# Performance work log

Hardware: AMD Instinct MI355X
Metric: run time of the kernel (lower is better)

Reference implementation:

```python
import jax, jax.numpy as jnp
import numpy as np

B, N = 32, 512            # batch, max nodes per graph
F_DIM, M_DIM = 1024, 256  # node feature dim, first hidden dim
N_SEM = 8                 # number of semantic-class experts
XYZ, DIM_E = 3, 8
OUT_SIZE = 2 * XYZ + DIM_E  # 14 (default reg branch)
EPS = 1e-8                # padding value used by out_seq_to_batch


def setup_inputs() -> dict:
    key = jax.random.key(0)
    ks = jax.random.split(key, 12)
    def w(k, shape, fan_in):
        return jax.random.normal(k, shape, jnp.float32) / np.float32(np.sqrt(fan_in))
    return {
        "nodes": jax.random.normal(ks[0], (B, N, F_DIM), jnp.float32),
        "sem": jax.random.randint(ks[1], (B, N), 0, N_SEM, jnp.int32),
        "lengths": jax.random.randint(ks[2], (B,), 64, N + 1, jnp.int32),
        # y expert MLPs (4 layers), stacked over experts
        "W1": w(ks[3], (N_SEM, F_DIM, M_DIM), F_DIM), "b1": jnp.zeros((N_SEM, M_DIM), jnp.float32),
        "W2": w(ks[4], (N_SEM, M_DIM, 64), M_DIM),   "b2": jnp.zeros((N_SEM, 64), jnp.float32),
        "W3": w(ks[5], (N_SEM, 64, 32), 64),         "b3": jnp.zeros((N_SEM, 32), jnp.float32),
        "W4": w(ks[6], (N_SEM, 32, OUT_SIZE), 32),   "b4": jnp.zeros((N_SEM, OUT_SIZE), jnp.float32),
        # rot expert MLPs (2 layers), stacked over experts
        "R1": w(ks[7], (N_SEM, F_DIM, M_DIM), F_DIM), "rb1": jnp.zeros((N_SEM, M_DIM), jnp.float32),
        "R2": w(ks[8], (N_SEM, M_DIM, XYZ), M_DIM),   "rb2": jnp.zeros((N_SEM, XYZ), jnp.float32),
    }


def _prim_mlps(nodes, sem, lengths, W1, b1, W2, b2, W3, b3, W4, b4, R1, rb1, R2, rb2):
    Bn, Nn, Fd = nodes.shape
    x = nodes.reshape(-1, Fd)                       # [T, F], T = B*N tokens
    semf = sem.reshape(-1)                          # [T] expert id per token
    # dense dispatch: run every expert on all tokens, then select per token
    h1 = jax.nn.relu(jnp.einsum('tf,efm->etm', x, W1) + b1[:, None, :])   # [E,T,M]
    h2 = jax.nn.relu(jnp.einsum('etm,emh->eth', h1, W2) + b2[:, None, :]) # [E,T,64]
    h3 = jax.nn.relu(jnp.einsum('eth,ehg->etg', h2, W3) + b3[:, None, :]) # [E,T,32]
    y_all = jnp.einsum('etg,ego->eto', h3, W4) + b4[:, None, :]           # [E,T,OUT]
    r1 = jax.nn.relu(jnp.einsum('tf,efm->etm', x, R1) + rb1[:, None, :])  # [E,T,M]
    rot_all = jnp.einsum('etm,emo->eto', r1, R2) + rb2[:, None, :]        # [E,T,XYZ]
    t = jnp.arange(x.shape[0])
    y = y_all[semf, t]                              # [T, OUT]
    rot = rot_all[semf, t]                          # [T, XYZ]
    out = jnp.concatenate([y, rot], axis=-1).reshape(Bn, Nn, -1)
    # positions beyond each graph's length are filled with eps (out_seq_to_batch)
    mask = (jnp.arange(Nn)[None, :] < lengths[:, None])[:, :, None]
    return jnp.where(mask, out, jnp.float32(EPS))


def reference(nodes, sem, lengths, W1, b1, W2, b2, W3, b3, W4, b4, R1, rb1, R2, rb2):
    return _prim_mlps(nodes, sem, lengths, W1, b1, W2, b2, W3, b3, W4, b4,
                      R1, rb1, R2, rb2)
```

## Files before the change

### kernel.cpp

```cpp
#include <hip/hip_runtime.h>
#include <stdint.h>

#define T_TOK 16384
#define NE 8
#define EPSV 1e-8f
#define MAXC128 136
#define MAXC64  264

#define WS_PERM   0
#define WS_PART   65536
#define WS_OFFS   67584
#define WS_XS     131072
#define WS_WT     (WS_XS + 16512*1024*2)
#define WS_H1     (WS_WT + 8*512*1024*2)
#define WS_W2T    (WS_H1 + 16448*512*2)
#define WS_W3T    (WS_W2T + 8*64*256*2)
#define WS_W4T    (WS_W3T + 8*32*64*2)
#define WS_R2T    (WS_W4T + 8*16*32*2)

typedef __attribute__((ext_vector_type(8))) short bf16x8;
typedef __attribute__((ext_vector_type(4))) float f32x4;

__device__ __forceinline__ unsigned short f2bf(float f) {
    unsigned u = __float_as_uint(f);
    u += 0x7fffu + ((u >> 16) & 1u);
    return (unsigned short)(u >> 16);
}
__device__ __forceinline__ float bf2f(unsigned short h) {
    return __uint_as_float(((unsigned)h) << 16);
}

__device__ __forceinline__ void gl_lds16(const void* g, void* l) {
    __builtin_amdgcn_global_load_lds(
        (const __attribute__((address_space(1))) void*)g,
        (__attribute__((address_space(3))) void*)l,
        16, 0, 0);
}

__device__ __forceinline__ bool chunk_lookup(const int* __restrict__ offs, int c, int csize,
                                             int& e, int& base, int& len) {
    int acc = 0;
#pragma unroll
    for (int i = 0; i < NE; i++) {
        int s = offs[i], t = offs[i + 1];
        int cc = (t - s + csize - 1) / csize;
        if (c < acc + cc) {
            e = i;
            base = s + (c - acc) * csize;
            len = (t - base < csize) ? (t - base) : csize;
            return true;
        }
        acc += cc;
    }
    return false;
}

__global__ __launch_bounds__(256) void k_hist(const int* __restrict__ sem, int* __restrict__ ws_i) {
    __shared__ int cnt[NE];
    int tid = threadIdx.x, lane = tid & 63;
    if (tid < NE) cnt[tid] = 0;
    __syncthreads();
    int s = sem[blockIdx.x * 256 + tid];
#pragma unroll
    for (int e = 0; e < NE; e++) {
        unsigned long long m = __ballot(s == e);
        if (lane == e) atomicAdd(&cnt[e], (int)__popcll(m));
    }
    __syncthreads();
    if (tid < NE) ws_i[(WS_PART >> 2) + blockIdx.x * NE + tid] = cnt[tid];
}

__global__ __launch_bounds__(256) void k_scatter(const int* __restrict__ sem, int* __restrict__ ws_i) {
    __shared__ int parts[64 * NE];
    __shared__ int tot[NE], preb[NE], ebase[NE + 1];
    __shared__ int cur[NE];
    int b = blockIdx.x, tid = threadIdx.x, lane = tid & 63;
    parts[tid] = ws_i[(WS_PART >> 2) + tid];
    parts[256 + tid] = ws_i[(WS_PART >> 2) + 256 + tid];
    __syncthreads();
    if (tid < NE) {
        int t = 0, p = 0;
        for (int bb = 0; bb < 64; bb++) {
            int v = parts[bb * NE + tid];
            t += v;
            if (bb < b) p += v;
        }
        tot[tid] = t; preb[tid] = p;
    }
    __syncthreads();
    if (tid == 0) {
        int base = 0;
        for (int e = 0; e < NE; e++) { ebase[e] = base; base += tot[e]; }
        ebase[NE] = base;
        if (b == 0)
            for (int e = 0; e <= NE; e++) ws_i[(WS_OFFS >> 2) + e] = ebase[e];
    }
    __syncthreads();
    if (tid < NE) cur[tid] = ebase[tid] + preb[tid];
    __syncthreads();
    int i = b * 256 + tid;
    int s = sem[i];
    int* perm = ws_i + (WS_PERM >> 2);
#pragma unroll
    for (int e = 0; e < NE; e++) {
        unsigned long long m = __ballot(s == e);
        if (s == e) {
            int leader = (int)__builtin_ctzll(m);
            int rank = (int)__popcll(m & ((1ull << lane) - 1ull));
            int bpos = 0;
            if (lane == leader) bpos = atomicAdd(&cur[e], (int)__popcll(m));
            bpos = __shfl(bpos, leader, 64);
            perm[bpos + rank] = i;
        }
    }
}

__global__ __launch_bounds__(256) void k_xgather(const float* __restrict__ x,
                                                 const int* __restrict__ perm,
                                                 unsigned short* __restrict__ xs) {
    int gid = blockIdx.x * 256 + threadIdx.x;
    int st = gid >> 7;
    int k8 = gid & 127;
    int src = perm[st];
    const float4* p = (const float4*)(x + (size_t)src * 1024 + k8 * 8);
    float4 a = p[0], b = p[1];
    unsigned r0 = (unsigned)f2bf(a.x) | ((unsigned)f2bf(a.y) << 16);
    unsigned r1 = (unsigned)f2bf(a.z) | ((unsigned)f2bf(a.w) << 16);
    unsigned r2 = (unsigned)f2bf(b.x) | ((unsigned)f2bf(b.y) << 16);
    unsigned r3 = (unsigned)f2bf(b.z) | ((unsigned)f2bf(b.w) << 16);
    *(uint4*)(xs + (size_t)st * 1024 + k8 * 8) = make_uint4(r0, r1, r2, r3);
}

__global__ __launch_bounds__(256) void k_wcvt(const float* __restrict__ W1,
                                              const float* __restrict__ R1,
                                              const float* __restrict__ W2,
                                              const float* __restrict__ W3,
                                              const float* __restrict__ W4,
                                              const float* __restrict__ R2,
                                              unsigned short* __restrict__ wt,
                                              unsigned short* __restrict__ w2t,
                                              unsigned short* __restrict__ w3t,
                                              unsigned short* __restrict__ w4t,
                                              unsigned short* __restrict__ r2t) {
    __shared__ float tile[64][65];
    int k0 = blockIdx.x * 64;
    int n0 = blockIdx.y * 64;
    int e  = blockIdx.z;
    const float* src = (n0 < 256) ? (W1 + (size_t)e * 1024 * 256 + n0)
                                  : (R1 + (size_t)e * 1024 * 256 + (n0 - 256));
    int tid = threadIdx.x;
    int rr = tid >> 4;
    int cg = (tid & 15) * 4;
#pragma unroll
    for (int p = 0; p < 4; p++) {
        int kk = p * 16 + rr;
        float4 v = *(const float4*)(src + (size_t)(k0 + kk) * 256 + cg);
        tile[kk][cg] = v.x; tile[kk][cg + 1] = v.y; tile[kk][cg + 2] = v.z; tile[kk][cg + 3] = v.w;
    }
    __syncthreads();
    int nn = tid >> 3;
    int k8 = tid & 7;
#pragma unroll
    for (int p = 0; p < 2; p++) {
        int n = p * 32 + nn;
        unsigned w[4];
#pragma unroll
        for (int j = 0; j < 4; j++) {
            float f0 = tile[k8 * 8 + 2 * j][n];
            float f1 = tile[k8 * 8 + 2 * j + 1][n];
            w[j] = (unsigned)f2bf(f0) | ((unsigned)f2bf(f1) << 16);
        }
        *(uint4*)(wt + (size_t)(e * 512 + n0 + n) * 1024 + k0 + k8 * 8) =
            make_uint4(w[0], w[1], w[2], w[3]);
    }
    if (blockIdx.y == 0) {
        int x = blockIdx.x;
        for (int j = tid; j < 1024; j += 256) {
            int idx = x * 1024 + j; int k = idx & 255, n = idx >> 8;
            w2t[(size_t)(e * 64 + n) * 256 + k] = f2bf(W2[(size_t)e * 16384 + k * 64 + n]);
        }
        if (tid < 128) {
            int idx = x * 128 + tid; int k = idx & 63, n = idx >> 6;
            w3t[(size_t)(e * 32 + n) * 64 + k] = f2bf(W3[(size_t)e * 2048 + k * 32 + n]);
        }
        if (tid < 32) {
            int idx = x * 32 + tid; int k = idx & 31, n = idx >> 5;
            w4t[(size_t)(e * 16 + n) * 32 + k] = (n < 14) ? f2bf(W4[(size_t)e * 448 + k * 14 + n])
                                                          : (unsigned short)0;
        }
        {
            int idx = x * 256 + tid; int k = idx & 255, n = idx >> 8;
            r2t[(size_t)(e * 16 + n) * 256 + k] = (n < 3) ? f2bf(R2[(size_t)e * 768 + k * 3 + n])
                                                          : (unsigned short)0;
        }
    }
}

__global__ __launch_bounds__(256) void k_gemm(const unsigned short* __restrict__ xs,
                                              const unsigned short* __restrict__ wt,
                                              const float* __restrict__ b1,
                                              const float* __restrict__ rb1,
                                              const int* __restrict__ ws_i,
                                              unsigned short* __restrict__ h1) {
    __shared__ __align__(16) short As[128 * 64];
    __shared__ __align__(16) short Bs[128 * 64];
    int e, base, len;
    if (!chunk_lookup(ws_i + (WS_OFFS >> 2), blockIdx.x, 128, e, base, len)) return;
    int n0 = blockIdx.y * 128;
    int tid = threadIdx.x;
    int wave = tid >> 6, lane = tid & 63;
    int quad = lane >> 4, lr = lane & 15;
    int wm = (wave & 1) * 64, wn = (wave >> 1) * 64;

    f32x4 acc[4][4];
#pragma unroll
    for (int i = 0; i < 4; i++)
#pragma unroll
        for (int j = 0; j < 4; j++) acc[i][j] = (f32x4){0.f, 0.f, 0.f, 0.f};

    const unsigned short* Ag = xs + (size_t)base * 1024;
    const unsigned short* Bg = wt + (size_t)(e * 512 + n0) * 1024;

    const unsigned short* srcA[4];
    const unsigned short* srcB[4];
    int dst[4];
#pragma unroll
    for (int i = 0; i < 4; i++) {
        int s = i * 256 + wave * 64 + lane;
        int r = s >> 3, c = s & 7;
        int cs = c ^ (r & 7);
        srcA[i] = Ag + (size_t)r * 1024 + cs * 8;
        srcB[i] = Bg + (size_t)r * 1024 + cs * 8;
        dst[i] = (i * 256 + wave * 64) * 8;
    }

    for (int kb = 0; kb < 16; kb++) {
        __syncthreads();
#pragma unroll
        for (int i = 0; i < 4; i++) {
            gl_lds16(srcA[i] + kb * 64, As + dst[i]);
            gl_lds16(srcB[i] + kb * 64, Bs + dst[i]);
        }
        __syncthreads();

        bf16x8 af[2][4], bfr[2][4];
#pragma unroll
        for (int im = 0; im < 4; im++) {
            int r = wm + im * 16 + lr;
#pragma unroll
            for (int kh = 0; kh < 2; kh++) {
                int q = kh * 4 + quad;
                af[kh][im] = *(const bf16x8*)(As + (r * 8 + (q ^ (r & 7))) * 8);
            }
        }
#pragma unroll
        for (int in = 0; in < 4; in++) {
            int r = wn + in * 16 + lr;
#pragma unroll
            for (int kh = 0; kh < 2; kh++) {
                int q = kh * 4 + quad;
                bfr[kh][in] = *(const bf16x8*)(Bs + (r * 8 + (q ^ (r & 7))) * 8);
            }
        }
#pragma unroll
        for (int kh = 0; kh < 2; kh++)
#pragma unroll
            for (int im = 0; im < 4; im++)
#pragma unroll
                for (int in = 0; in < 4; in++)
                    acc[im][in] = __builtin_amdgcn_mfma_f32_16x16x32_bf16(af[kh][im], bfr[kh][in], acc[im][in], 0, 0, 0);
    }

#pragma unroll
    for (int in = 0; in < 4; in++) {
        int gcol = n0 + wn + in * 16 + lr;
        float bias = (gcol < 256) ? b1[e * 256 + gcol] : rb1[e * 256 + gcol - 256];
#pragma unroll
        for (int im = 0; im < 4; im++) {
#pragma unroll
            for (int v = 0; v < 4; v++) {
                int r = wm + im * 16 + quad * 4 + v;
                if (r < len) {
                    float val = fmaxf(acc[im][in][v] + bias, 0.f);
                    h1[(size_t)(base + r) * 512 + gcol] = f2bf(val);
                }
            }
        }
    }
}

__global__ __launch_bounds__(256) void k_tail(const unsigned short* __restrict__ h1,
                                              const int* __restrict__ ws_i,
                                              const unsigned short* __restrict__ w2t,
                                              const unsigned short* __restrict__ w3t,
                                              const unsigned short* __restrict__ w4t,
                                              const unsigned short* __restrict__ r2t,
                                              const float* __restrict__ b2,
                                              const float* __restrict__ b3,
                                              const float* __restrict__ b4,
                                              const float* __restrict__ rb2,
                                              const int* __restrict__ lengths,
                                              float* __restrict__ out) {
    __shared__ __align__(16) unsigned short h2s[4][16][64];
    __shared__ __align__(16) unsigned short h3s[4][16][32];

    int e, base, len;
    if (!chunk_lookup(ws_i + (WS_OFFS >> 2), blockIdx.x, 64, e, base, len)) return;
    int tid = threadIdx.x, wave = tid >> 6, lane = tid & 63;
    int quad = lane >> 4, lr = lane & 15;
    int m0 = wave * 16;

    const unsigned short* Ap = h1 + (size_t)(base + m0) * 512;

    f32x4 acc2[4];
#pragma unroll
    for (int t = 0; t < 4; t++) {
        float bb = b2[e * 64 + t * 16 + lr];
        acc2[t] = (f32x4){bb, bb, bb, bb};
    }
    f32x4 accr;
    { float bb = (lr < 3) ? rb2[e * 3 + lr] : 0.f; accr = (f32x4){bb, bb, bb, bb}; }

    const unsigned short* W2e = w2t + (size_t)e * 64 * 256;
    const unsigned short* R2e = r2t + (size_t)e * 16 * 256;
#pragma unroll
    for (int kk = 0; kk < 8; kk++) {
        int k0 = kk * 32;
        bf16x8 a = *(const bf16x8*)(Ap + lr * 512 + k0 + quad * 8);
#pragma unroll
        for (int t = 0; t < 4; t++) {
            bf16x8 b = *(const bf16x8*)(W2e + (t * 16 + lr) * 256 + k0 + quad * 8);
            acc2[t] = __builtin_amdgcn_mfma_f32_16x16x32_bf16(a, b, acc2[t], 0, 0, 0);
        }
        bf16x8 ar = *(const bf16x8*)(Ap + lr * 512 + 256 + k0 + quad * 8);
        bf16x8 br = *(const bf16x8*)(R2e + lr * 256 + k0 + quad * 8);
        accr = __builtin_amdgcn_mfma_f32_16x16x32_bf16(ar, br, accr, 0, 0, 0);
    }
#pragma unroll
    for (int t = 0; t < 4; t++)
#pragma unroll
        for (int v = 0; v < 4; v++)
            h2s[wave][quad * 4 + v][t * 16 + lr] = f2bf(fmaxf(acc2[t][v], 0.f));

    f32x4 acc3[2];
#pragma unroll
    for (int t = 0; t < 2; t++) {
        float bb = b3[e * 32 + t * 16 + lr];
        acc3[t] = (f32x4){bb, bb, bb, bb};
    }
    const unsigned short* W3e = w3t + (size_t)e * 32 * 64;
#pragma unroll
    for (int kk = 0; kk < 2; kk++) {
        int k0 = kk * 32;
        bf16x8 a = *(const bf16x8*)(&h2s[wave][lr][k0 + quad * 8]);
#pragma unroll
        for (int t = 0; t < 2; t++) {
            bf16x8 b = *(const bf16x8*)(W3e + (t * 16 + lr) * 64 + k0 + quad * 8);
            acc3[t] = __builtin_amdgcn_mfma_f32_16x16x32_bf16(a, b, acc3[t], 0, 0, 0);
        }
    }
#pragma unroll
    for (int t = 0; t < 2; t++)
#pragma unroll
        for (int v = 0; v < 4; v++)
            h3s[wave][quad * 4 + v][t * 16 + lr] = f2bf(fmaxf(acc3[t][v], 0.f));

    f32x4 acc4;
    { float bb = (lr < 14) ? b4[e * 14 + lr] : 0.f; acc4 = (f32x4){bb, bb, bb, bb}; }
    {
        bf16x8 a = *(const bf16x8*)(&h3s[wave][lr][quad * 8]);
        bf16x8 b = *(const bf16x8*)(w4t + ((size_t)e * 16 + lr) * 32 + quad * 8);
        acc4 = __builtin_amdgcn_mfma_f32_16x16x32_bf16(a, b, acc4, 0, 0, 0);
    }

    const int* perm = ws_i + (WS_PERM >> 2);
#pragma unroll
    for (int v = 0; v < 4; v++) {
        int t = m0 + quad * 4 + v;
        if (t < len) {
            int token = perm[base + t];
            int bi = token >> 9, ni = token & 511;
            int valid = ni < lengths[bi];
            if (lr < 14) out[(size_t)token * 17 + lr] = valid ? acc4[v] : EPSV;
            if (lr < 3)  out[(size_t)token * 17 + 14 + lr] = valid ? accr[v] : EPSV;
        }
    }
}

extern "C" void kernel_launch(void* const* d_in, const int* in_sizes, int n_in,
                              void* d_out, int out_size, void* d_ws, size_t ws_size,
                              hipStream_t stream) {
    (void)in_sizes; (void)n_in; (void)out_size; (void)ws_size;
    const float* nodes   = (const float*)d_in[0];
    const int*   sem     = (const int*)d_in[1];
    const int*   lengths = (const int*)d_in[2];
    const float* W1 = (const float*)d_in[3];
    const float* b1 = (const float*)d_in[4];
    const float* W2 = (const float*)d_in[5];
    const float* b2 = (const float*)d_in[6];
    const float* W3 = (const float*)d_in[7];
    const float* b3 = (const float*)d_in[8];
    const float* W4 = (const float*)d_in[9];
    const float* b4 = (const float*)d_in[10];
    const float* R1  = (const float*)d_in[11];
    const float* rb1 = (const float*)d_in[12];
    const float* R2  = (const float*)d_in[13];
    const float* rb2 = (const float*)d_in[14];
    float* out = (float*)d_out;

    char* ws = (char*)d_ws;
    int* ws_i = (int*)ws;
    unsigned short* xs  = (unsigned short*)(ws + WS_XS);
    unsigned short* wt  = (unsigned short*)(ws + WS_WT);
    unsigned short* h1  = (unsigned short*)(ws + WS_H1);
    unsigned short* w2t = (unsigned short*)(ws + WS_W2T);
    unsigned short* w3t = (unsigned short*)(ws + WS_W3T);
    unsigned short* w4t = (unsigned short*)(ws + WS_W4T);
    unsigned short* r2t = (unsigned short*)(ws + WS_R2T);

    hipLaunchKernelGGL(k_hist, dim3(64), dim3(256), 0, stream, sem, ws_i);
    hipLaunchKernelGGL(k_scatter, dim3(64), dim3(256), 0, stream, sem, ws_i);
    hipLaunchKernelGGL(k_xgather, dim3(8192), dim3(256), 0, stream, nodes, (const int*)ws_i, xs);
    hipLaunchKernelGGL(k_wcvt, dim3(16, 8, 8), dim3(256), 0, stream,
                       W1, R1, W2, W3, W4, R2, wt, w2t, w3t, w4t, r2t);
    hipLaunchKernelGGL(k_gemm, dim3(MAXC128, 4), dim3(256), 0, stream,
                       (const unsigned short*)xs, (const unsigned short*)wt, b1, rb1,
                       (const int*)ws_i, h1);
    hipLaunchKernelGGL(k_tail, dim3(MAXC64), dim3(256), 0, stream,
                       (const unsigned short*)h1, (const int*)ws_i,
                       (const unsigned short*)w2t, (const unsigned short*)w3t,
                       (const unsigned short*)w4t, (const unsigned short*)r2t,
                       b2, b3, b4, rb2, lengths, out);
}
```

Before: 204.2 us.

## Fuse token gather and bf16 conversion into GEMM A-tile loads; merge prep kernels

Drops the separate gather kernel, which wrote a permuted bf16 copy of the node features. The first-layer GEMM now reads fp32 rows straight from the input through the permutation, converts them to bf16 in registers and stores them into LDS. The histogram and weight-conversion kernels are merged into one launch, so there are fewer launches and the 32MB intermediate write and reread are gone. The cost is that each of the 4 N-tile blocks re-reads the fp32 A rows, doubling A bytes per load compared with bf16. A is now loaded synchronously through registers instead of asynchronously with global_load_lds.

Result: slower. 213.4 us (+4.5%).

```diff
diff --git a/kernel.cpp b/kernel.cpp
--- a/kernel.cpp
+++ b/kernel.cpp
@@ -10,8 +10,7 @@
 #define WS_PERM   0
 #define WS_PART   65536
 #define WS_OFFS   67584
-#define WS_XS     131072
-#define WS_WT     (WS_XS + 16512*1024*2)
+#define WS_WT     131072
 #define WS_H1     (WS_WT + 8*512*1024*2)
 #define WS_W2T    (WS_H1 + 16448*512*2)
 #define WS_W3T    (WS_W2T + 8*64*256*2)
@@ -25,9 +24,6 @@
     unsigned u = __float_as_uint(f);
     u += 0x7fffu + ((u >> 16) & 1u);
     return (unsigned short)(u >> 16);
-}
-__device__ __forceinline__ float bf2f(unsigned short h) {
-    return __uint_as_float(((unsigned)h) << 16);
 }
 
 __device__ __forceinline__ void gl_lds16(const void* g, void* l) {
@@ -55,19 +51,86 @@
     return false;
 }
 
-__global__ __launch_bounds__(256) void k_hist(const int* __restrict__ sem, int* __restrict__ ws_i) {
-    __shared__ int cnt[NE];
-    int tid = threadIdx.x, lane = tid & 63;
-    if (tid < NE) cnt[tid] = 0;
+__global__ __launch_bounds__(256) void k_prep1(const float* __restrict__ W1,
+                                               const float* __restrict__ R1,
+                                               const float* __restrict__ W2,
+                                               const float* __restrict__ W3,
+                                               const float* __restrict__ W4,
+                                               const float* __restrict__ R2,
+                                               const int* __restrict__ sem,
+                                               unsigned short* __restrict__ wt,
+                                               unsigned short* __restrict__ w2t,
+                                               unsigned short* __restrict__ w3t,
+                                               unsigned short* __restrict__ w4t,
+                                               unsigned short* __restrict__ r2t,
+                                               int* __restrict__ ws_i) {
+    __shared__ float tile[64][65];
+    int id = blockIdx.x, tid = threadIdx.x;
+    if (id >= 1024) {
+        __shared__ int cnt[NE];
+        int hb = id - 1024, lane = tid & 63;
+        if (tid < NE) cnt[tid] = 0;
+        __syncthreads();
+        int s = sem[hb * 256 + tid];
+#pragma unroll
+        for (int e = 0; e < NE; e++) {
+            unsigned long long m = __ballot(s == e);
+            if (lane == e) atomicAdd(&cnt[e], (int)__popcll(m));
+        }
+        __syncthreads();
+        if (tid < NE) ws_i[(WS_PART >> 2) + hb * NE + tid] = cnt[tid];
+        return;
+    }
+    int e = id >> 7, rem = id & 127;
+    int ny = rem >> 4, kx = rem & 15;
+    int k0 = kx * 64, n0 = ny * 64;
+    const float* src = (n0 < 256) ? (W1 + (size_t)e * 1024 * 256 + n0)
+                                  : (R1 + (size_t)e * 1024 * 256 + (n0 - 256));
+    int rr = tid >> 4;
+    int cg = (tid & 15) * 4;
+#pragma unroll
+    for (int p = 0; p < 4; p++) {
+        int kk = p * 16 + rr;
+        float4 v = *(const float4*)(src + (size_t)(k0 + kk) * 256 + cg);
+        tile[kk][cg] = v.x; tile[kk][cg + 1] = v.y; tile[kk][cg + 2] = v.z; tile[kk][cg + 3] = v.w;
+    }
     __syncthreads();
-    int s = sem[blockIdx.x * 256 + tid];
-#pragma unroll
-    for (int e = 0; e < NE; e++) {
-        unsigned long long m = __ballot(s == e);
-        if (lane == e) atomicAdd(&cnt[e], (int)__popcll(m));
-    }
-    __syncthreads();
-    if (tid < NE) ws_i[(WS_PART >> 2) + blockIdx.x * NE + tid] = cnt[tid];
+    int nn = tid >> 3;
+    int k8 = tid & 7;
+#pragma unroll
+    for (int p = 0; p < 2; p++) {
+        int n = p * 32 + nn;
+        unsigned w[4];
+#pragma unroll
+        for (int j = 0; j < 4; j++) {
+            float f0 = tile[k8 * 8 + 2 * j][n];
+            float f1 = tile[k8 * 8 + 2 * j + 1][n];
+            w[j] = (unsigned)f2bf(f0) | ((unsigned)f2bf(f1) << 16);
+        }
+        *(uint4*)(wt + (size_t)(e * 512 + n0 + n) * 1024 + k0 + k8 * 8) =
+            make_uint4(w[0], w[1], w[2], w[3]);
+    }
+    if (ny == 0) {
+        int x = kx;
+        for (int j = tid; j < 1024; j += 256) {
+            int idx = x * 1024 + j; int k = idx & 255, n = idx >> 8;
+            w2t[(size_t)(e * 64 + n) * 256 + k] = f2bf(W2[(size_t)e * 16384 + k * 64 + n]);
+        }
+        if (tid < 128) {
+            int idx = x * 128 + tid; int k = idx & 63, n = idx >> 6;
+            w3t[(size_t)(e * 32 + n) * 64 + k] = f2bf(W3[(size_t)e * 2048 + k * 32 + n]);
+        }
+        if (tid < 32) {
+            int idx = x * 32 + tid; int k = idx & 31, n = idx >> 5;
+            w4t[(size_t)(e * 16 + n) * 32 + k] = (n < 14) ? f2bf(W4[(size_t)e * 448 + k * 14 + n])
+                                                          : (unsigned short)0;
+        }
+        {
+            int idx = x * 256 + tid; int k = idx & 255, n = idx >> 8;
+            r2t[(size_t)(e * 16 + n) * 256 + k] = (n < 3) ? f2bf(R2[(size_t)e * 768 + k * 3 + n])
+                                                          : (unsigned short)0;
+        }
+    }
 }
 
 __global__ __launch_bounds__(256) void k_scatter(const int* __restrict__ sem, int* __restrict__ ws_i) {
@@ -115,88 +178,7 @@
     }
 }
 
-__global__ __launch_bounds__(256) void k_xgather(const float* __restrict__ x,
-                                                 const int* __restrict__ perm,
-                                                 unsigned short* __restrict__ xs) {
-    int gid = blockIdx.x * 256 + threadIdx.x;
-    int st = gid >> 7;
-    int k8 = gid & 127;
-    int src = perm[st];
-    const float4* p = (const float4*)(x + (size_t)src * 1024 + k8 * 8);
-    float4 a = p[0], b = p[1];
-    unsigned r0 = (unsigned)f2bf(a.x) | ((unsigned)f2bf(a.y) << 16);
-    unsigned r1 = (unsigned)f2bf(a.z) | ((unsigned)f2bf(a.w) << 16);
-    unsigned r2 = (unsigned)f2bf(b.x) | ((unsigned)f2bf(b.y) << 16);
-    unsigned r3 = (unsigned)f2bf(b.z) | ((unsigned)f2bf(b.w) << 16);
-    *(uint4*)(xs + (size_t)st * 1024 + k8 * 8) = make_uint4(r0, r1, r2, r3);
-}
-
-__global__ __launch_bounds__(256) void k_wcvt(const float* __restrict__ W1,
-                                              const float* __restrict__ R1,
-                                              const float* __restrict__ W2,
-                                              const float* __restrict__ W3,
-                                              const float* __restrict__ W4,
-                                              const float* __restrict__ R2,
-                                              unsigned short* __restrict__ wt,
-                                              unsigned short* __restrict__ w2t,
-                                              unsigned short* __restrict__ w3t,
-                                              unsigned short* __restrict__ w4t,
-                                              unsigned short* __restrict__ r2t) {
-    __shared__ float tile[64][65];
-    int k0 = blockIdx.x * 64;
-    int n0 = blockIdx.y * 64;
-    int e  = blockIdx.z;
-    const float* src = (n0 < 256) ? (W1 + (size_t)e * 1024 * 256 + n0)
-                                  : (R1 + (size_t)e * 1024 * 256 + (n0 - 256));
-    int tid = threadIdx.x;
-    int rr = tid >> 4;
-    int cg = (tid & 15) * 4;
-#pragma unroll
-    for (int p = 0; p < 4; p++) {
-        int kk = p * 16 + rr;
-        float4 v = *(const float4*)(src + (size_t)(k0 + kk) * 256 + cg);
-        tile[kk][cg] = v.x; tile[kk][cg + 1] = v.y; tile[kk][cg + 2] = v.z; tile[kk][cg + 3] = v.w;
-    }
-    __syncthreads();
-    int nn = tid >> 3;
-    int k8 = tid & 7;
-#pragma unroll
-    for (int p = 0; p < 2; p++) {
-        int n = p * 32 + nn;
-        unsigned w[4];
-#pragma unroll
-        for (int j = 0; j < 4; j++) {
-            float f0 = tile[k8 * 8 + 2 * j][n];
-            float f1 = tile[k8 * 8 + 2 * j + 1][n];
-            w[j] = (unsigned)f2bf(f0) | ((unsigned)f2bf(f1) << 16);
-        }
-        *(uint4*)(wt + (size_t)(e * 512 + n0 + n) * 1024 + k0 + k8 * 8) =
-            make_uint4(w[0], w[1], w[2], w[3]);
-    }
-    if (blockIdx.y == 0) {
-        int x = blockIdx.x;
-        for (int j = tid; j < 1024; j += 256) {
-            int idx = x * 1024 + j; int k = idx & 255, n = idx >> 8;
-            w2t[(size_t)(e * 64 + n) * 256 + k] = f2bf(W2[(size_t)e * 16384 + k * 64 + n]);
-        }
-        if (tid < 128) {
-            int idx = x * 128 + tid; int k = idx & 63, n = idx >> 6;
-            w3t[(size_t)(e * 32 + n) * 64 + k] = f2bf(W3[(size_t)e * 2048 + k * 32 + n]);
-        }
-        if (tid < 32) {
-            int idx = x * 32 + tid; int k = idx & 31, n = idx >> 5;
-            w4t[(size_t)(e * 16 + n) * 32 + k] = (n < 14) ? f2bf(W4[(size_t)e * 448 + k * 14 + n])
-                                                          : (unsigned short)0;
-        }
-        {
-            int idx = x * 256 + tid; int k = idx & 255, n = idx >> 8;
-            r2t[(size_t)(e * 16 + n) * 256 + k] = (n < 3) ? f2bf(R2[(size_t)e * 768 + k * 3 + n])
-                                                          : (unsigned short)0;
-        }
-    }
-}
-
-__global__ __launch_bounds__(256) void k_gemm(const unsigned short* __restrict__ xs,
+__global__ __launch_bounds__(256) void k_gemm(const float* __restrict__ nodes,
                                               const unsigned short* __restrict__ wt,
                                               const float* __restrict__ b1,
                                               const float* __restrict__ rb1,
@@ -211,6 +193,7 @@
     int wave = tid >> 6, lane = tid & 63;
     int quad = lane >> 4, lr = lane & 15;
     int wm = (wave & 1) * 64, wn = (wave >> 1) * 64;
+    const int* perm = ws_i + (WS_PERM >> 2);
 
     f32x4 acc[4][4];
 #pragma unroll
@@ -218,28 +201,38 @@
 #pragma unroll
         for (int j = 0; j < 4; j++) acc[i][j] = (f32x4){0.f, 0.f, 0.f, 0.f};
 
-    const unsigned short* Ag = xs + (size_t)base * 1024;
     const unsigned short* Bg = wt + (size_t)(e * 512 + n0) * 1024;
 
-    const unsigned short* srcA[4];
+    int cs = (tid & 7) ^ ((tid >> 3) & 7);
+    const float* srcA[4];
     const unsigned short* srcB[4];
-    int dst[4];
+    int dstA[4], dstB[4];
 #pragma unroll
     for (int i = 0; i < 4; i++) {
+        int R = i * 32 + (tid >> 3);
+        int row = base + R; if (row > T_TOK - 1) row = T_TOK - 1;
+        srcA[i] = nodes + (size_t)perm[row] * 1024 + cs * 8;
+        dstA[i] = (i * 256 + tid) * 8;
         int s = i * 256 + wave * 64 + lane;
-        int r = s >> 3, c = s & 7;
-        int cs = c ^ (r & 7);
-        srcA[i] = Ag + (size_t)r * 1024 + cs * 8;
-        srcB[i] = Bg + (size_t)r * 1024 + cs * 8;
-        dst[i] = (i * 256 + wave * 64) * 8;
+        int r = s >> 3, cb = (s & 7) ^ (r & 7);
+        srcB[i] = Bg + (size_t)r * 1024 + cb * 8;
+        dstB[i] = (i * 256 + wave * 64) * 8;
     }
 
     for (int kb = 0; kb < 16; kb++) {
         __syncthreads();
 #pragma unroll
+        for (int i = 0; i < 4; i++)
+            gl_lds16(srcB[i] + kb * 64, Bs + dstB[i]);
+#pragma unroll
         for (int i = 0; i < 4; i++) {
-            gl_lds16(srcA[i] + kb * 64, As + dst[i]);
-            gl_lds16(srcB[i] + kb * 64, Bs + dst[i]);
+            const float4* p = (const float4*)(srcA[i] + kb * 64);
+            float4 a = p[0], b = p[1];
+            unsigned r0 = (unsigned)f2bf(a.x) | ((unsigned)f2bf(a.y) << 16);
+            unsigned r1 = (unsigned)f2bf(a.z) | ((unsigned)f2bf(a.w) << 16);
+            unsigned r2 = (unsigned)f2bf(b.x) | ((unsigned)f2bf(b.y) << 16);
+            unsigned r3 = (unsigned)f2bf(b.z) | ((unsigned)f2bf(b.w) << 16);
+            *(uint4*)(As + dstA[i]) = make_uint4(r0, r1, r2, r3);
         }
         __syncthreads();
 
@@ -410,7 +403,6 @@
 
     char* ws = (char*)d_ws;
     int* ws_i = (int*)ws;
-    unsigned short* xs  = (unsigned short*)(ws + WS_XS);
     unsigned short* wt  = (unsigned short*)(ws + WS_WT);
     unsigned short* h1  = (unsigned short*)(ws + WS_H1);
     unsigned short* w2t = (unsigned short*)(ws + WS_W2T);
@@ -418,14 +410,11 @@
     unsigned short* w4t = (unsigned short*)(ws + WS_W4T);
     unsigned short* r2t = (unsigned short*)(ws + WS_R2T);
 
-    hipLaunchKernelGGL(k_hist, dim3(64), dim3(256), 0, stream, sem, ws_i);
+    hipLaunchKernelGGL(k_prep1, dim3(1088), dim3(256), 0, stream,
+                       W1, R1, W2, W3, W4, R2, sem, wt, w2t, w3t, w4t, r2t, ws_i);
     hipLaunchKernelGGL(k_scatter, dim3(64), dim3(256), 0, stream, sem, ws_i);
-    hipLaunchKernelGGL(k_xgather, dim3(8192), dim3(256), 0, stream, nodes, (const int*)ws_i, xs);
-    hipLaunchKernelGGL(k_wcvt, dim3(16, 8, 8), dim3(256), 0, stream,
-                       W1, R1, W2, W3, W4, R2, wt, w2t, w3t, w4t, r2t);
     hipLaunchKernelGGL(k_gemm, dim3(MAXC128, 4), dim3(256), 0, stream,
-                       (const unsigned short*)xs, (const unsigned short*)wt, b1, rb1,
-                       (const int*)ws_i, h1);
+                       nodes, (const unsigned short*)wt, b1, rb1, (const int*)ws_i, h1);
     hipLaunchKernelGGL(k_tail, dim3(MAXC64), dim3(256), 0, stream,
                        (const unsigned short*)h1, (const int*)ws_i,
                        (const unsigned short*)w2t, (const unsigned short*)w3t,
```
